# Optimization experiments

Measured on AMD Instinct MI355X. Metric: run time of the kernel, lower is better.

The kernel has to match this reference:

```python
import jax, jax.numpy as jnp
import numpy as np
import math

D_MODEL = 512
NHEAD = 8
D_K = D_MODEL // NHEAD
FACTOR = 5


def setup_inputs() -> dict:
    key = jax.random.key(0)
    ks = jax.random.split(key, 9)
    B, L = 2, 2048
    s = 1.0 / math.sqrt(D_MODEL)
    inp = {
        "x": jax.random.normal(ks[0], (B, L, D_MODEL), dtype=jnp.float32),
        "Wq": jax.random.normal(ks[1], (D_MODEL, D_MODEL), dtype=jnp.float32) * s,
        "bq": jnp.zeros((D_MODEL,), dtype=jnp.float32),
        "Wk": jax.random.normal(ks[2], (D_MODEL, D_MODEL), dtype=jnp.float32) * s,
        "bk": jnp.zeros((D_MODEL,), dtype=jnp.float32),
        "Wv": jax.random.normal(ks[3], (D_MODEL, D_MODEL), dtype=jnp.float32) * s,
        "bv": jnp.zeros((D_MODEL,), dtype=jnp.float32),
        "Wo": jax.random.normal(ks[4], (D_MODEL, D_MODEL), dtype=jnp.float32) * s,
        "bo": jnp.zeros((D_MODEL,), dtype=jnp.float32),
    }
    return inp


def reference(x, Wq, bq, Wk, bk, Wv, bv, Wo, bo):
    B, L, _ = x.shape
    # u keys kept per query (static: depends only on static L)
    u = min(L, int(FACTOR * math.log(L)) if L > 1 else L)

    def proj(W, b):
        # [B,L,D] -> [B,H,L,d_k]
        y = x @ W.T + b
        return y.reshape(B, L, NHEAD, D_K).transpose(0, 2, 1, 3)

    Q = proj(Wq, bq)
    K = proj(Wk, bk)
    V = proj(Wv, bv)

    scores = jnp.einsum("bhqd,bhkd->bhqk", Q, K) / math.sqrt(D_K)  # [B,H,L,L]
    # topk thresholding: keep only scores >= u-th largest per query row
    topk_vals, _ = jax.lax.top_k(scores, u)
    thresh = topk_vals[..., -1:]
    scores = jnp.where(scores < thresh, -10000.0, scores)
    attn = jax.nn.softmax(scores, axis=-1)  # dropout disabled (p=0 / eval)
    out = jnp.einsum("bhqk,bhkd->bhqd", attn, V)  # [B,H,L,d_k]
    out = out.transpose(0, 2, 1, 3).reshape(B, L, D_MODEL)
    return out @ Wo.T + bo
```

## Files before the change

### kernel.cpp

```cpp
#include <hip/hip_runtime.h>
#include <hip/hip_fp16.h>
#include <math.h>

#define LSEQ   2048
#define DMODEL 512
#define NHEAD  8
#define DK     64
#define UK     38

typedef __attribute__((ext_vector_type(8))) _Float16 v8h;
typedef __attribute__((ext_vector_type(4))) _Float16 v4h;
typedef __attribute__((ext_vector_type(4))) float    v4f;

__device__ __forceinline__ unsigned long long mapu64(double x){
    unsigned long long s = (unsigned long long)__double_as_longlong(x);
    return (s & 0x8000000000000000ull) ? ~s : (s | 0x8000000000000000ull);
}
__device__ __forceinline__ unsigned map32(float x){
    unsigned s = __float_as_uint(x);
    return (s & 0x80000000u) ? ~s : (s | 0x80000000u);
}
__device__ __forceinline__ float unmap32(unsigned u){
    unsigned s = (u & 0x80000000u) ? (u & 0x7fffffffu) : ~u;
    return __uint_as_float(s);
}
__device__ __forceinline__ unsigned map16(unsigned h){
    return (h & 0x8000u) ? ((~h) & 0xFFFFu) : (h | 0x8000u);
}

__global__ __launch_bounds__(256) void split_hl(
    const float* __restrict__ X,  const float* __restrict__ Wq,
    const float* __restrict__ Wk, const float* __restrict__ Wv,
    _Float16* __restrict__ Xh, _Float16* __restrict__ Xl,
    _Float16* __restrict__ Whl)
{
    const int idx = blockIdx.x * 256 + threadIdx.x;
    const int NXQ = (4096 * 512) / 4;
    const float* __restrict__ src;
    _Float16* __restrict__ dh;
    _Float16* __restrict__ dl;
    size_t off;
    if (idx < NXQ){
        src = X; dh = Xh; dl = Xl; off = (size_t)idx * 4;
    } else {
        int wi = idx - NXQ;
        int m  = wi >> 16;
        src = (m == 0) ? Wq : (m == 1 ? Wk : Wv);
        dh  = Whl + (size_t)m * 524288;
        dl  = dh + 262144;
        off = (size_t)(wi & 65535) * 4;
    }
    float4 v = *(const float4*)&src[off];
    v4h h, l;
    h[0] = (_Float16)v.x; l[0] = (_Float16)(v.x - (float)h[0]);
    h[1] = (_Float16)v.y; l[1] = (_Float16)(v.y - (float)h[1]);
    h[2] = (_Float16)v.z; l[2] = (_Float16)(v.z - (float)h[2]);
    h[3] = (_Float16)v.w; l[3] = (_Float16)(v.w - (float)h[3]);
    *(v4h*)&dh[off] = h;
    *(v4h*)&dl[off] = l;
}

__global__ __launch_bounds__(256) void qkv_f16(
    const _Float16* __restrict__ Xh, const _Float16* __restrict__ Xl,
    const _Float16* __restrict__ Whl,
    const float* __restrict__ bq, const float* __restrict__ bk,
    const float* __restrict__ bv,
    double* __restrict__ qD, double* __restrict__ kRow,
    __half* __restrict__ qH, __half* __restrict__ kH, float* __restrict__ vB)
{
    const int mode = blockIdx.z;
    const _Float16* __restrict__ Wh = Whl + (size_t)mode * 524288;
    const _Float16* __restrict__ Wl = Wh + 262144;
    const float* __restrict__ bias = (mode == 0) ? bq : (mode == 1 ? bk : bv);
    const int r0 = blockIdx.x * 64, c0 = blockIdx.y * 64;
    __shared__ _Float16 Ah[64][72], Al[64][72];
    __shared__ _Float16 Bh[64][72], Bl[64][72];
    const int tid  = threadIdx.x;
    const int lane = tid & 63, wv = tid >> 6;
    const int m0   = wv << 4;
    const int row  = lane & 15, kq = lane >> 4;

    v4f acc[4] = {};

    for (int kb = 0; kb < DMODEL; kb += 64){
        __syncthreads();
        #pragma unroll
        for (int it = 0; it < 2; ++it){
            int slot = it * 256 + tid;
            int m = slot >> 3, o8 = (slot & 7) << 3;
            size_t ga = (size_t)(r0 + m) * DMODEL + kb + o8;
            size_t gb = (size_t)(c0 + m) * DMODEL + kb + o8;
            *(v8h*)&Ah[m][o8] = *(const v8h*)&Xh[ga];
            *(v8h*)&Al[m][o8] = *(const v8h*)&Xl[ga];
            *(v8h*)&Bh[m][o8] = *(const v8h*)&Wh[gb];
            *(v8h*)&Bl[m][o8] = *(const v8h*)&Wl[gb];
        }
        __syncthreads();
        v8h ah0 = *(const v8h*)&Ah[m0 + row][kq * 8];
        v8h ah1 = *(const v8h*)&Ah[m0 + row][kq * 8 + 32];
        v8h al0 = *(const v8h*)&Al[m0 + row][kq * 8];
        v8h al1 = *(const v8h*)&Al[m0 + row][kq * 8 + 32];
        #pragma unroll
        for (int j = 0; j < 4; ++j){
            const int j0 = j << 4;
            v8h bh0 = *(const v8h*)&Bh[j0 + row][kq * 8];
            v8h bh1 = *(const v8h*)&Bh[j0 + row][kq * 8 + 32];
            v8h bl0 = *(const v8h*)&Bl[j0 + row][kq * 8];
            v8h bl1 = *(const v8h*)&Bl[j0 + row][kq * 8 + 32];
            acc[j] = __builtin_amdgcn_mfma_f32_16x16x32_f16(ah0, bh0, acc[j], 0, 0, 0);
            acc[j] = __builtin_amdgcn_mfma_f32_16x16x32_f16(ah0, bl0, acc[j], 0, 0, 0);
            acc[j] = __builtin_amdgcn_mfma_f32_16x16x32_f16(al0, bh0, acc[j], 0, 0, 0);
            acc[j] = __builtin_amdgcn_mfma_f32_16x16x32_f16(ah1, bh1, acc[j], 0, 0, 0);
            acc[j] = __builtin_amdgcn_mfma_f32_16x16x32_f16(ah1, bl1, acc[j], 0, 0, 0);
            acc[j] = __builtin_amdgcn_mfma_f32_16x16x32_f16(al1, bh1, acc[j], 0, 0, 0);
        }
    }

    const int h = c0 >> 6;
    #pragma unroll
    for (int j = 0; j < 4; ++j){
        const int dk = (j << 4) + row;
        const float bi = bias[c0 + dk];
        #pragma unroll
        for (int rr = 0; rr < 4; ++rr){
            const int r = r0 + m0 + (kq << 2) + rr;
            const int bidx = r >> 11, l = r & 2047;
            const size_t rowb = (size_t)(bidx * NHEAD + h) * LSEQ + l;
            float v = acc[j][rr] + bi;
            if (mode == 0){
                double vd = (double)v * 0.125;
                qD[rowb * DK + dk] = vd;
                ((_Float16*)qH)[rowb * DK + dk] = (_Float16)vd;
            } else if (mode == 1){
                kRow[rowb * DK + dk] = (double)v;
                ((_Float16*)kH)[rowb * DK + dk] = (_Float16)v;
            } else {
                vB[rowb * DK + dk] = v;
            }
        }
    }
}

__global__ __launch_bounds__(256) void gemm_f32(
    const float* __restrict__ X, const float* __restrict__ W,
    const float* __restrict__ bias, float* __restrict__ out)
{
    const int r0 = blockIdx.x * 64, c0 = blockIdx.y * 64;
    __shared__ float Xs[32][68];
    __shared__ float Ws[32][68];
    const int tid = threadIdx.x;
    const int tx = tid & 15, ty = tid >> 4;
    float acc[4][4] = {};
    for (int kb = 0; kb < DMODEL; kb += 32){
        __syncthreads();
        #pragma unroll
        for (int i = 0; i < 2; ++i){
            int f4 = i * 256 + tid;
            int m = f4 >> 3, kg = (f4 & 7) << 2;
            float4 xv = *(const float4*)&X[(r0 + m) * DMODEL + kb + kg];
            Xs[kg+0][m] = xv.x; Xs[kg+1][m] = xv.y; Xs[kg+2][m] = xv.z; Xs[kg+3][m] = xv.w;
            float4 wv = *(const float4*)&W[(c0 + m) * DMODEL + kb + kg];
            Ws[kg+0][m] = wv.x; Ws[kg+1][m] = wv.y; Ws[kg+2][m] = wv.z; Ws[kg+3][m] = wv.w;
        }
        __syncthreads();
        #pragma unroll
        for (int kk = 0; kk < 32; ++kk){
            float4 av = *(const float4*)&Xs[kk][ty << 2];
            float4 bv = *(const float4*)&Ws[kk][tx << 2];
            float a[4] = {av.x, av.y, av.z, av.w};
            float b[4] = {bv.x, bv.y, bv.z, bv.w};
            #pragma unroll
            for (int ii = 0; ii < 4; ++ii)
                #pragma unroll
                for (int jj = 0; jj < 4; ++jj)
                    acc[ii][jj] = fmaf(a[ii], b[jj], acc[ii][jj]);
        }
    }
    #pragma unroll
    for (int ii = 0; ii < 4; ++ii){
        int r = r0 + (ty << 2) + ii;
        float4 o;
        o.x = acc[ii][0] + bias[c0 + (tx << 2) + 0];
        o.y = acc[ii][1] + bias[c0 + (tx << 2) + 1];
        o.z = acc[ii][2] + bias[c0 + (tx << 2) + 2];
        o.w = acc[ii][3] + bias[c0 + (tx << 2) + 3];
        *(float4*)&out[(size_t)r * DMODEL + c0 + (tx << 2)] = o;
    }
}

__global__ __launch_bounds__(256) void score_gemm(
    const __half* __restrict__ qH, const __half* __restrict__ kH,
    __half* __restrict__ Sh, const int bh0)
{
    const int bh = bh0 + blockIdx.z;
    const int r0 = blockIdx.x * 128, c0 = blockIdx.y * 128;
    __shared__ _Float16 Qs[128][72];
    __shared__ _Float16 Ks[128][72];
    const int tid = threadIdx.x;
    const int lane = tid & 63, wv = tid >> 6;
    const size_t qb = ((size_t)bh * LSEQ + r0) * DK;
    const size_t kb = ((size_t)bh * LSEQ + c0) * DK;
    #pragma unroll
    for (int i = 0; i < 4; ++i){
        int c = i * 256 + tid;
        int m = c >> 3, off8 = (c & 7) << 3;
        *(v8h*)&Qs[m][off8] = *(const v8h*)&qH[qb + (size_t)m * DK + off8];
        *(v8h*)&Ks[m][off8] = *(const v8h*)&kH[kb + (size_t)m * DK + off8];
    }
    __syncthreads();
    const int m0 = (wv >> 1) << 6;
    const int n0 = (wv & 1) << 6;
    const int row = lane & 15, kq = lane >> 4;
    v8h a0[4], a1[4], b0[4], b1[4];
    #pragma unroll
    for (int r = 0; r < 4; ++r){
        a0[r] = *(const v8h*)&Qs[m0 + r*16 + row][kq * 8];
        a1[r] = *(const v8h*)&Qs[m0 + r*16 + row][kq * 8 + 32];
    }
    #pragma unroll
    for (int c = 0; c < 4; ++c){
        b0[c] = *(const v8h*)&Ks[n0 + c*16 + row][kq * 8];
        b1[c] = *(const v8h*)&Ks[n0 + c*16 + row][kq * 8 + 32];
    }
    #pragma unroll
    for (int r = 0; r < 4; ++r){
        #pragma unroll
        for (int c = 0; c < 4; ++c){
            v4f acc = {0.f, 0.f, 0.f, 0.f};
            acc = __builtin_amdgcn_mfma_f32_16x16x32_f16(a0[r], b0[c], acc, 0, 0, 0);
            acc = __builtin_amdgcn_mfma_f32_16x16x32_f16(a1[r], b1[c], acc, 0, 0, 0);
            #pragma unroll
            for (int i = 0; i < 4; ++i){
                int gr = r0 + m0 + r*16 + kq*4 + i;
                int gc = c0 + n0 + c*16 + row;
                Sh[((size_t)blockIdx.z * LSEQ + gr) * LSEQ + gc] = (__half)acc[i];
            }
        }
    }
}

__device__ __forceinline__ void finish_common(
    const int ncand, const int gl, const int bh, const int lane,
    const double qd, const double* __restrict__ kRow, const float* __restrict__ vB,
    float* __restrict__ ctx, int* __restrict__ jlsR, float* __restrict__ wlsR,
    double* __restrict__ sLds)
{
    const unsigned long long mlt = (1ull << lane) - 1ull;
    if (lane >= ncand) jlsR[lane] = 0;
    if (lane < 4) jlsR[64 + lane] = 0;
    int myJ = jlsR[lane];

    double q8[8];
    #pragma unroll
    for (int k = 0; k < 8; ++k) q8[k] = __shfl(qd, (lane & 7) + (k << 3));
    const int grp = lane >> 3, dl = lane & 7;
    const size_t kb = (size_t)bh * LSEQ;
    for (int e0 = 0; e0 < ncand; e0 += 8){
        int j = jlsR[e0 + grp];
        const double* __restrict__ kr = &kRow[(kb + j) * DK + dl];
        double s = 0.0;
        #pragma unroll
        for (int k = 0; k < 8; ++k) s = fma(q8[k], kr[k << 3], s);
        s += __shfl_xor(s, 1); s += __shfl_xor(s, 2); s += __shfl_xor(s, 4);
        if (dl == 0) sLds[e0 + grp] = s;
    }
    double myS = (lane < ncand) ? sLds[lane] : -1.0e308;

    unsigned long long cu = (lane < ncand) ? mapu64(myS) : 0ull;
    unsigned long long T64 = 0ull;
    for (int bit = 63; bit >= 0; --bit){
        unsigned long long Tp = T64 | (1ull << bit);
        int c = __popcll(__ballot(cu >= Tp));
        if (c >= UK){ T64 = Tp; if (c == UK) break; }
    }
    const bool sel = (cu >= T64);

    double xm = sel ? myS : -1.0e308;
    #pragma unroll
    for (int off = 32; off; off >>= 1) xm = fmax(xm, __shfl_xor(xm, off));
    float w = sel ? expf((float)(myS - xm)) : 0.0f;
    float z = w;
    #pragma unroll
    for (int off = 32; off; off >>= 1) z += __shfl_xor(z, off);
    unsigned long long bm = __ballot(sel);
    int p = __popcll(bm & mlt);
    if (sel){ wlsR[p] = w; jlsR[p] = myJ; }
    const int cnt = __popcll(bm);
    const float invZ = 1.0f / z;

    if (lane >= cnt) wlsR[lane] = 0.0f;
    if (lane < 4){ wlsR[64 + lane] = 0.0f; jlsR[64 + lane] = 0; }

    const float* __restrict__ vsl = vB + (size_t)bh * (LSEQ * DK);
    float o = 0.0f;
    for (int e = 0; e < cnt; e += 4){
        float w0 = wlsR[e],   w1 = wlsR[e+1], w2 = wlsR[e+2], w3 = wlsR[e+3];
        int   j0 = jlsR[e],   j1 = jlsR[e+1], j2 = jlsR[e+2], j3 = jlsR[e+3];
        float v0 = vsl[(size_t)j0 * DK + lane];
        float v1 = vsl[(size_t)j1 * DK + lane];
        float v2 = vsl[(size_t)j2 * DK + lane];
        float v3 = vsl[(size_t)j3 * DK + lane];
        o = fmaf(w0, v0, o); o = fmaf(w1, v1, o);
        o = fmaf(w2, v2, o); o = fmaf(w3, v3, o);
    }
    ctx[((size_t)(bh >> 3) * LSEQ + gl) * DMODEL + (bh & 7) * DK + lane] = o * invZ;
}

__device__ __forceinline__ void finish_row_f32(
    float (&acc)[32], const int gl, const int bh, const int lane, const float margin,
    const double qd, const double* __restrict__ kRow, const float* __restrict__ vB,
    float* __restrict__ ctx, int* __restrict__ jlsR, float* __restrict__ wlsR,
    double* __restrict__ sLds)
{
    unsigned u[32];
    #pragma unroll
    for (int ch = 0; ch < 32; ++ch) u[ch] = map32(acc[ch]);
    unsigned T = 0u; int curc = 2048;
    for (int bit = 31; bit >= 0; --bit){
        unsigned Tp = T | (1u << bit);
        int c = 0;
        #pragma unroll
        for (int ch = 0; ch < 32; ++ch) c += __popcll(__ballot(u[ch] >= Tp));
        if (c >= UK){ T = Tp; curc = c; }
        if (curc <= 48) break;
    }
    const unsigned Tlo = map32(unmap32(T) - margin);
    const unsigned long long mlt = (1ull << lane) - 1ull;
    int base = 0;
    #pragma unroll
    for (int ch = 0; ch < 32; ++ch){
        bool sel = (u[ch] >= Tlo);
        unsigned long long bm = __ballot(sel);
        int p = base + __popcll(bm & mlt);
        if (sel && p < 64) jlsR[p] = (ch << 6) + lane;
        base += __popcll(bm);
    }
    const int ncand = base > 64 ? 64 : base;
    finish_common(ncand, gl, bh, lane, qd, kRow, vB, ctx, jlsR, wlsR, sLds);
}

__global__ __launch_bounds__(256) void select_kernel(
    const __half* __restrict__ Sh, const double* __restrict__ qD,
    const double* __restrict__ kRow, const float* __restrict__ vB,
    float* __restrict__ ctx, const int bh0)
{
    __shared__ int    jls[4][68];
    __shared__ float  wls[4][68];
    __shared__ double sds[4][64];
    const int tid = threadIdx.x, lane = tid & 63, wv = tid >> 6;
    const int rgS = blockIdx.x * 4 + wv;
    const int bh = bh0 + (rgS >> 11), l = rgS & 2047;
    const double qd = qD[((size_t)bh * LSEQ + l) * DK + lane];
    unsigned u[32];
    const unsigned short* __restrict__ Srow =
        (const unsigned short*)Sh + (size_t)rgS * LSEQ;
    #pragma unroll
    for (int it = 0; it < 4; ++it){
        uint4 v = *(const uint4*)&Srow[it * 512 + (lane << 3)];
        unsigned ws[4] = {v.x, v.y, v.z, v.w};
        #pragma unroll
        for (int q = 0; q < 4; ++q){
            u[it*8 + 2*q]     = map16(ws[q] & 0xFFFFu);
            u[it*8 + 2*q + 1] = map16(ws[q] >> 16);
        }
    }
    unsigned T = 0u; int curc = 2048;
    for (int bit = 15; bit >= 0; --bit){
        unsigned Tp = T | (1u << bit);
        int c = 0;
        #pragma unroll
        for (int ch = 0; ch < 32; ++ch) c += __popcll(__ballot(u[ch] >= Tp));
        if (c >= UK){ T = Tp; curc = c; }
        if (curc <= 48) break;
    }
    unsigned hb = (T & 0x8000u) ? (T & 0x7FFFu) : ((~T) & 0xFFFFu);
    float tf = __half2float(__ushort_as_half((unsigned short)hb)) - 2.2e-2f;
    unsigned short tlb = __half_as_ushort(__float2half_rd(tf));
    const unsigned Tlo = map16(tlb);

    const unsigned long long mlt = (1ull << lane) - 1ull;
    int base = 0;
    #pragma unroll
    for (int ch = 0; ch < 32; ++ch){
        bool sel = (u[ch] >= Tlo);
        unsigned long long bm = __ballot(sel);
        int p = base + __popcll(bm & mlt);
        int j = ((ch >> 3) << 9) + (lane << 3) + (ch & 7);
        if (sel && p < 64) jls[wv][p] = j;
        base += __popcll(bm);
    }
    const int ncand = base > 64 ? 64 : base;
    finish_common(ncand, l, bh, lane, qd, kRow, vB, ctx,
                  &jls[wv][0], &wls[wv][0], &sds[wv][0]);
}

__global__ __launch_bounds__(256) void attn_kernel(
    const double* __restrict__ qD, const double* __restrict__ kRow,
    const float* __restrict__ vB, float* __restrict__ ctx)
{
    __shared__ float2 Kld2[16 * 66];
    __shared__ float  qsf[8][64];
    __shared__ int    jls[8][68];
    __shared__ float  wlsf[8][68];
    __shared__ double sds[8][64];

    const int tid = threadIdx.x, lane = tid & 63, wv = tid >> 6;
    const int bh = blockIdx.x >> 8;
    const int l0 = (blockIdx.x & 255) << 3;
    const int rA = l0 + (wv << 1), rB = rA + 1;

    for (int e = tid; e < 512; e += 256){
        int r = e >> 6, d = e & 63;
        qsf[r][d] = (float)qD[((size_t)bh * LSEQ + l0 + r) * DK + d];
    }
    const double qdA = qD[((size_t)bh * LSEQ + rA) * DK + lane];
    const double qdB = qD[((size_t)bh * LSEQ + rB) * DK + lane];

    float accA[32] = {}, accB[32] = {};
    const size_t kBase = (size_t)bh * (LSEQ * DK);

    for (int dh = 0; dh < 2; ++dh){
        __syncthreads();
        float qa[32], qb[32];
        #pragma unroll
        for (int i = 0; i < 8; ++i){
            float4 va = *(const float4*)&qsf[wv << 1][dh * 32 + i * 4];
            qa[i*4+0]=va.x; qa[i*4+1]=va.y; qa[i*4+2]=va.z; qa[i*4+3]=va.w;
            float4 vb4 = *(const float4*)&qsf[(wv << 1) + 1][dh * 32 + i * 4];
            qb[i*4+0]=vb4.x; qb[i*4+1]=vb4.y; qb[i*4+2]=vb4.z; qb[i*4+3]=vb4.w;
        }
        #pragma unroll
        for (int ch = 0; ch < 32; ++ch){
            const int cb = ch << 6;
            __syncthreads();
            #pragma unroll
            for (int i = 0; i < 4; ++i){
                int j   = i * 16 + (wv << 2) + (lane >> 4);
                int dpl = lane & 15;
                double2 kd = *(const double2*)&kRow[kBase + (size_t)(cb + j) * DK + dh * 32 + dpl * 2];
                Kld2[dpl * 66 + j] = make_float2((float)kd.x, (float)kd.y);
            }
            __syncthreads();
            float a0 = accA[ch], b0 = accB[ch];
            #pragma unroll
            for (int dpl = 0; dpl < 16; ++dpl){
                float2 k = Kld2[dpl * 66 + lane];
                a0 = fmaf(qa[2*dpl],   k.x, a0);
                a0 = fmaf(qa[2*dpl+1], k.y, a0);
                b0 = fmaf(qb[2*dpl],   k.x, b0);
                b0 = fmaf(qb[2*dpl+1], k.y, b0);
            }
            accA[ch] = a0; accB[ch] = b0;
        }
    }

    finish_row_f32(accA, rA, bh, lane, 1e-3f, qdA, kRow, vB, ctx,
                   &jls[wv<<1][0], &wlsf[wv<<1][0], &sds[wv<<1][0]);
    finish_row_f32(accB, rB, bh, lane, 1e-3f, qdB, kRow, vB, ctx,
                   &jls[(wv<<1)+1][0], &wlsf[(wv<<1)+1][0], &sds[(wv<<1)+1][0]);
}

extern "C" void kernel_launch(void* const* d_in, const int* in_sizes, int n_in,
                              void* d_out, int out_size, void* d_ws, size_t ws_size,
                              hipStream_t stream)
{
    const float* x  = (const float*)d_in[0];
    const float* Wq = (const float*)d_in[1];
    const float* bq = (const float*)d_in[2];
    const float* Wk = (const float*)d_in[3];
    const float* bk = (const float*)d_in[4];
    const float* Wv = (const float*)d_in[5];
    const float* bv = (const float*)d_in[6];
    const float* Wo = (const float*)d_in[7];
    const float* bo = (const float*)d_in[8];
    float* out = (float*)d_out;
    char* ws = (char*)d_ws;
    const size_t MiB = 1024 * 1024;
    double* qD   = (double*)(ws);
    double* kRow = (double*)(ws + 16 * MiB);
    float*  vB   = (float*) (ws + 32 * MiB);
    float*  ctx  = (float*) (ws + 40 * MiB);
    __half* qH   = (__half*)(ws + 48 * MiB);
    __half* kH   = (__half*)(ws + 52 * MiB);
    __half* Sh   = (__half*)(ws + 56 * MiB);
    _Float16* Xh  = (_Float16*)(ws + 40 * MiB);
    _Float16* Xl  = (_Float16*)(ws + 44 * MiB);
    _Float16* Whl = (_Float16*)(ws + 56 * MiB);
    size_t avail = (ws_size > 56 * MiB) ? (ws_size - 56 * MiB) : 0;
    int slab = (int)(avail / (8 * MiB)); if (slab > 16) slab = 16;

    dim3 blk(256);
    split_hl<<<dim3(2816), blk, 0, stream>>>(x, Wq, Wk, Wv, Xh, Xl, Whl);
    qkv_f16 <<<dim3(64, 8, 3), blk, 0, stream>>>(Xh, Xl, Whl, bq, bk, bv,
                                                 qD, kRow, qH, kH, vB);
    if (slab >= 1){
        for (int s0 = 0; s0 < NHEAD * 2; s0 += slab){
            int nb = NHEAD * 2 - s0; if (nb > slab) nb = slab;
            score_gemm   <<<dim3(16, 16, nb), blk, 0, stream>>>(qH, kH, Sh, s0);
            select_kernel<<<dim3(nb * 512),   blk, 0, stream>>>(Sh, qD, kRow, vB, ctx, s0);
        }
    } else {
        attn_kernel<<<dim3(4096), blk, 0, stream>>>(qD, kRow, vB, ctx);
    }
    gemm_f32<<<dim3(64, 8), blk, 0, stream>>>(ctx, Wo, bo, out);
}
```

Before: 271.0 us.

## Use split-fp16 MFMA for output projection and stage score tile stores

Replaces the scalar fp32 output projection with an hi/lo fp16 split of ctx and Wo, followed by an MFMA GEMM using three products per k-step to keep near-fp32 accuracy. Separately, score_gemm now writes its 128x128 fp16 tile to shared memory first and then stores it to global as coalesced 16-byte rows, replacing scattered 2-byte stores. This adds an extra split kernel pass and its memory traffic, and reuses the workspace regions that held qH/kH and Sh.

```diff
diff --git a/kernel.cpp b/kernel.cpp
--- a/kernel.cpp
+++ b/kernel.cpp
@@ -11,6 +11,7 @@
 typedef __attribute__((ext_vector_type(8))) _Float16 v8h;
 typedef __attribute__((ext_vector_type(4))) _Float16 v4h;
 typedef __attribute__((ext_vector_type(4))) float    v4f;
+typedef __attribute__((ext_vector_type(8))) unsigned short v8us;
 
 __device__ __forceinline__ unsigned long long mapu64(double x){
     unsigned long long s = (unsigned long long)__double_as_longlong(x);
@@ -60,6 +61,33 @@
     *(v4h*)&dl[off] = l;
 }
 
+__global__ __launch_bounds__(256) void split_ctx(
+    const float* __restrict__ ctx, const float* __restrict__ Wo,
+    _Float16* __restrict__ Ch, _Float16* __restrict__ Cl,
+    _Float16* __restrict__ WoH, _Float16* __restrict__ WoL)
+{
+    const int idx = blockIdx.x * 256 + threadIdx.x;
+    const int NCQ = (4096 * 512) / 4;
+    const float* __restrict__ src;
+    _Float16* __restrict__ dh;
+    _Float16* __restrict__ dl;
+    size_t off;
+    if (idx < NCQ){
+        src = ctx; dh = Ch; dl = Cl; off = (size_t)idx * 4;
+    } else {
+        src = Wo; dh = WoH; dl = WoL;
+        off = (size_t)(idx - NCQ) * 4;
+    }
+    float4 v = *(const float4*)&src[off];
+    v4h h, l;
+    h[0] = (_Float16)v.x; l[0] = (_Float16)(v.x - (float)h[0]);
+    h[1] = (_Float16)v.y; l[1] = (_Float16)(v.y - (float)h[1]);
+    h[2] = (_Float16)v.z; l[2] = (_Float16)(v.z - (float)h[2]);
+    h[3] = (_Float16)v.w; l[3] = (_Float16)(v.w - (float)h[3]);
+    *(v4h*)&dh[off] = h;
+    *(v4h*)&dl[off] = l;
+}
+
 __global__ __launch_bounds__(256) void qkv_f16(
     const _Float16* __restrict__ Xh, const _Float16* __restrict__ Xl,
     const _Float16* __restrict__ Whl,
@@ -141,6 +169,67 @@
     }
 }
 
+__global__ __launch_bounds__(256) void o_proj(
+    const _Float16* __restrict__ Ch, const _Float16* __restrict__ Cl,
+    const _Float16* __restrict__ WoH, const _Float16* __restrict__ WoL,
+    const float* __restrict__ bias, float* __restrict__ out)
+{
+    const int r0 = blockIdx.x * 64, c0 = blockIdx.y * 64;
+    __shared__ _Float16 Ah[64][72], Al[64][72];
+    __shared__ _Float16 Bh[64][72], Bl[64][72];
+    const int tid  = threadIdx.x;
+    const int lane = tid & 63, wv = tid >> 6;
+    const int m0   = wv << 4;
+    const int row  = lane & 15, kq = lane >> 4;
+
+    v4f acc[4] = {};
+
+    for (int kb = 0; kb < DMODEL; kb += 64){
+        __syncthreads();
+        #pragma unroll
+        for (int it = 0; it < 2; ++it){
+            int slot = it * 256 + tid;
+            int m = slot >> 3, o8 = (slot & 7) << 3;
+            size_t ga = (size_t)(r0 + m) * DMODEL + kb + o8;
+            size_t gb = (size_t)(c0 + m) * DMODEL + kb + o8;
+            *(v8h*)&Ah[m][o8] = *(const v8h*)&Ch[ga];
+            *(v8h*)&Al[m][o8] = *(const v8h*)&Cl[ga];
+            *(v8h*)&Bh[m][o8] = *(const v8h*)&WoH[gb];
+            *(v8h*)&Bl[m][o8] = *(const v8h*)&WoL[gb];
+        }
+        __syncthreads();
+        v8h ah0 = *(const v8h*)&Ah[m0 + row][kq * 8];
+        v8h ah1 = *(const v8h*)&Ah[m0 + row][kq * 8 + 32];
+        v8h al0 = *(const v8h*)&Al[m0 + row][kq * 8];
+        v8h al1 = *(const v8h*)&Al[m0 + row][kq * 8 + 32];
+        #pragma unroll
+        for (int j = 0; j < 4; ++j){
+            const int j0 = j << 4;
+            v8h bh0 = *(const v8h*)&Bh[j0 + row][kq * 8];
+            v8h bh1 = *(const v8h*)&Bh[j0 + row][kq * 8 + 32];
+            v8h bl0 = *(const v8h*)&Bl[j0 + row][kq * 8];
+            v8h bl1 = *(const v8h*)&Bl[j0 + row][kq * 8 + 32];
+            acc[j] = __builtin_amdgcn_mfma_f32_16x16x32_f16(ah0, bh0, acc[j], 0, 0, 0);
+            acc[j] = __builtin_amdgcn_mfma_f32_16x16x32_f16(ah0, bl0, acc[j], 0, 0, 0);
+            acc[j] = __builtin_amdgcn_mfma_f32_16x16x32_f16(al0, bh0, acc[j], 0, 0, 0);
+            acc[j] = __builtin_amdgcn_mfma_f32_16x16x32_f16(ah1, bh1, acc[j], 0, 0, 0);
+            acc[j] = __builtin_amdgcn_mfma_f32_16x16x32_f16(ah1, bl1, acc[j], 0, 0, 0);
+            acc[j] = __builtin_amdgcn_mfma_f32_16x16x32_f16(al1, bh1, acc[j], 0, 0, 0);
+        }
+    }
+
+    #pragma unroll
+    for (int j = 0; j < 4; ++j){
+        const int dk = (j << 4) + row;
+        const float bi = bias[c0 + dk];
+        #pragma unroll
+        for (int rr = 0; rr < 4; ++rr){
+            const int r = r0 + m0 + (kq << 2) + rr;
+            out[(size_t)r * DMODEL + c0 + dk] = acc[j][rr] + bi;
+        }
+    }
+}
+
 __global__ __launch_bounds__(256) void gemm_f32(
     const float* __restrict__ X, const float* __restrict__ W,
     const float* __restrict__ bias, float* __restrict__ out)
@@ -194,8 +283,10 @@
 {
     const int bh = bh0 + blockIdx.z;
     const int r0 = blockIdx.x * 128, c0 = blockIdx.y * 128;
-    __shared__ _Float16 Qs[128][72];
-    __shared__ _Float16 Ks[128][72];
+    __shared__ _Float16 smem[2 * 128 * 72];
+    _Float16 (*Qs)[72] = (_Float16(*)[72])smem;
+    _Float16 (*Ks)[72] = (_Float16(*)[72])(smem + 128 * 72);
+    unsigned short (*Cs)[136] = (unsigned short(*)[136])smem;
     const int tid = threadIdx.x;
     const int lane = tid & 63, wv = tid >> 6;
     const size_t qb = ((size_t)bh * LSEQ + r0) * DK;
@@ -222,6 +313,7 @@
         b0[c] = *(const v8h*)&Ks[n0 + c*16 + row][kq * 8];
         b1[c] = *(const v8h*)&Ks[n0 + c*16 + row][kq * 8 + 32];
     }
+    __syncthreads();
     #pragma unroll
     for (int r = 0; r < 4; ++r){
         #pragma unroll
@@ -231,11 +323,19 @@
             acc = __builtin_amdgcn_mfma_f32_16x16x32_f16(a1[r], b1[c], acc, 0, 0, 0);
             #pragma unroll
             for (int i = 0; i < 4; ++i){
-                int gr = r0 + m0 + r*16 + kq*4 + i;
-                int gc = c0 + n0 + c*16 + row;
-                Sh[((size_t)blockIdx.z * LSEQ + gr) * LSEQ + gc] = (__half)acc[i];
+                Cs[m0 + r*16 + kq*4 + i][n0 + c*16 + row] =
+                    (unsigned short)__half_as_ushort((__half)acc[i]);
             }
         }
+    }
+    __syncthreads();
+    unsigned short* __restrict__ dst =
+        (unsigned short*)Sh + ((size_t)blockIdx.z * LSEQ + r0) * LSEQ + c0;
+    #pragma unroll
+    for (int g0 = 0; g0 < 8; ++g0){
+        int g = g0 * 256 + tid;
+        int rr = g >> 4, cg = (g & 15) << 3;
+        *(v8us*)&dst[(size_t)rr * LSEQ + cg] = *(const v8us*)&Cs[rr][cg];
     }
 }
 
@@ -486,6 +586,10 @@
     _Float16* Xh  = (_Float16*)(ws + 40 * MiB);
     _Float16* Xl  = (_Float16*)(ws + 44 * MiB);
     _Float16* Whl = (_Float16*)(ws + 56 * MiB);
+    _Float16* Ch  = (_Float16*)(ws + 48 * MiB);
+    _Float16* Cl  = (_Float16*)(ws + 52 * MiB);
+    _Float16* WoH = (_Float16*)(ws + 56 * MiB);
+    _Float16* WoL = (_Float16*)(ws + 56 * MiB + 512 * 1024);
     size_t avail = (ws_size > 56 * MiB) ? (ws_size - 56 * MiB) : 0;
     int slab = (int)(avail / (8 * MiB)); if (slab > 16) slab = 16;
 
@@ -499,8 +603,10 @@
             score_gemm   <<<dim3(16, 16, nb), blk, 0, stream>>>(qH, kH, Sh, s0);
             select_kernel<<<dim3(nb * 512),   blk, 0, stream>>>(Sh, qD, kRow, vB, ctx, s0);
         }
+        split_ctx<<<dim3(2304), blk, 0, stream>>>(ctx, Wo, Ch, Cl, WoH, WoL);
+        o_proj  <<<dim3(64, 8), blk, 0, stream>>>(Ch, Cl, WoH, WoL, bo, out);
     } else {
         attn_kernel<<<dim3(4096), blk, 0, stream>>>(qD, kRow, vB, ctx);
-    }
-    gemm_f32<<<dim3(64, 8), blk, 0, stream>>>(ctx, Wo, bo, out);
-}
+        gemm_f32<<<dim3(64, 8), blk, 0, stream>>>(ctx, Wo, bo, out);
+    }
+}
```

Result: faster. 251.7 us (median of 3 runs) (-7.1%).
